# Optimization experiments

Measured on AMD Instinct MI355X. Metric: run time of the kernel, lower is better.

## Reference

```python
import jax, jax.numpy as jnp
import numpy as np

QKV_DIM = 256
C = 32
N_HEAD = 8
OUT_DIM = 256
B1, B2, N = 1, 128, 256


def setup_inputs() -> dict:
    key = jax.random.key(0)
    ks = jax.random.split(key, 8)
    hc = N_HEAD * C
    return {
        "in_data": jax.random.normal(ks[0], (B1, B2, N, QKV_DIM), jnp.float32),
        "mask": jnp.ones((B1, B2, N), jnp.float32),
        "nonbatched_bias": jax.random.normal(ks[1], (B1, N_HEAD, N, N), jnp.float32),
        "w_qkv": jax.random.normal(ks[2], (3 * hc, QKV_DIM), jnp.float32) * (1.0 / np.sqrt(QKV_DIM)),
        "w_gate": jax.random.normal(ks[3], (hc, QKV_DIM), jnp.float32) * 0.02,
        "gating_bias": jnp.ones((hc,), jnp.float32),
        "w_o": jax.random.normal(ks[4], (OUT_DIM, hc), jnp.float32) * 0.02,
        "b_o": jnp.zeros((OUT_DIM,), jnp.float32),
    }


def reference(in_data, mask, nonbatched_bias, w_qkv, w_gate, gating_bias, w_o, b_o):
    scaling = C ** (-0.5)
    # fused QKV projection: [b1,b2,n,3*h*c]
    qkv = jnp.einsum("abnd,ed->abne", in_data, w_qkv)
    q, k, v = jnp.split(qkv, 3, axis=-1)

    def to_heads(t):  # b1 b2 n (h d) -> b1 b2 h n d
        b1, b2, n, _ = t.shape
        return t.reshape(b1, b2, n, N_HEAD, C).transpose(0, 1, 3, 2, 4)

    q, k, v = to_heads(q) * scaling, to_heads(k), to_heads(v)
    # logits: [b1,b2,h,q,k]
    logits = jnp.einsum("abhqd,abhkd->abhqk", q, k)
    mask_bias = (mask[:, :, None, None, :] - 1.0) * 1e9
    logits = logits + mask_bias + nonbatched_bias[:, None]  # broadcast bias over b2
    weights = jax.nn.softmax(logits, axis=-1)
    weighted_avg = jnp.einsum("abhqk,abhkd->abhqd", weights, v)
    b1, b2, h, n, d = weighted_avg.shape
    weighted_avg = weighted_avg.transpose(0, 1, 3, 2, 4).reshape(b1, b2, n, h * d)
    # sigmoid gating
    gate = jax.nn.sigmoid(jnp.einsum("abnd,ed->abne", in_data, w_gate) + gating_bias)
    weighted_avg = gate * weighted_avg
    return jnp.einsum("abne,oe->abno", weighted_avg, w_o) + b_o
```

## Files before the change

### kernel.cpp

```cpp
#include <hip/hip_runtime.h>
#include <hip/hip_bf16.h>
#include <math.h>

#define B2      128
#define NSEQ    256
#define DMODEL  256
#define NHEAD   8
#define CDIM    32
#define HC      256
#define NROWS   (B2*NSEQ)
#define SCALING 0.17677669529663687f

typedef __attribute__((ext_vector_type(8))) short bf16x8;
typedef __attribute__((ext_vector_type(4))) float f32x4;

static __device__ __forceinline__ ushort f2bf(float f) {
    __hip_bfloat16 b = __float2bfloat16(f);
    ushort r; __builtin_memcpy(&r, &b, 2); return r;
}
static __device__ __forceinline__ ushort f2bf_fast(float f) {
    uint u = __builtin_bit_cast(uint, f);
    return (ushort)((u + 0x8000u) >> 16);
}
static __device__ __forceinline__ uint fpack2(float a, float b) {
    const uint ua = __builtin_bit_cast(uint, a) + 0x8000u;
    const uint ub = __builtin_bit_cast(uint, b) + 0x8000u;
    return (ua >> 16) | (ub & 0xFFFF0000u);
}
static __device__ __forceinline__ float bf2f(ushort u) {
    __hip_bfloat16 b; __builtin_memcpy(&b, &u, 2); return __bfloat162float(b);
}
static __device__ __forceinline__ void gload_lds16(const void* g, void* l) {
    __builtin_amdgcn_global_load_lds((const __attribute__((address_space(1))) void*)g,
                                     (__attribute__((address_space(3))) void*)l, 16, 0, 0);
}

#define SWZ(c) ((((c) >> 2) & 3) << 5)

__global__ __launch_bounds__(256) void convertW_kernel(
    const float* __restrict__ Wqkv, const float* __restrict__ Wg,
    const float* __restrict__ Wo,
    ushort* __restrict__ wqkvgb, ushort* __restrict__ wob)
{
    const int NQ = 196608 / 4, NG = 65536 / 4, NO = 65536 / 4;
    const int idx = blockIdx.x * 256 + threadIdx.x;
    const float* src; ushort* dst; int off; float scale = 1.0f;
    if (idx < NQ)           { src = Wqkv; dst = wqkvgb;          off = idx;
                              if (off < 16384) scale = SCALING; }
    else if (idx < NQ + NG) { src = Wg;   dst = wqkvgb + 196608; off = idx - NQ; }
    else                    { src = Wo;   dst = wob;             off = idx - NQ - NG; }
    float4 v = ((const float4*)src)[off];
    union { ushort u[4]; uint2 q; } p;
    p.u[0] = f2bf(v.x * scale); p.u[1] = f2bf(v.y * scale);
    p.u[2] = f2bf(v.z * scale); p.u[3] = f2bf(v.w * scale);
    *(uint2*)(dst + (size_t)off * 4) = p.q;
}

__global__ __launch_bounds__(512, 4) void fused_attn_kernel(
    const float* __restrict__ X,
    const ushort* __restrict__ Wb,
    const float* __restrict__ gbias,
    const float* __restrict__ bias,
    const float* __restrict__ mask,
    ushort* __restrict__ wa_ws)
{
    __shared__ ushort S[40960];

    const int tid  = threadIdx.x;
    const int sid  = (blockIdx.x & 7) * 128 + (blockIdx.x >> 3);
    const int b2   = sid >> 3;
    const int h    = sid & 7;
    const int w    = tid >> 6;
    const int lane = tid & 63;
    const int lj   = lane & 15;
    const int lg   = lane >> 4;
    const int xsl  = ((lg ^ ((lj >> 1) & 3)) << 3);

    {
        const int row  = tid >> 2;
        const int slot = tid & 3;
        const int g8   = (slot ^ ((row >> 1) & 3)) * 8;
        const int wrow = (row < 96) ? ((row >> 5) * 256 + h * 32 + (row & 31))
                                    : (768 + h * 32 + (row & 31));
        const ushort* wsrc = Wb + (size_t)wrow * 256 + g8;
        char* wdst = (char*)S + row * 64 + slot * 16;
        #pragma unroll
        for (int c = 0; c < 8; ++c)
            gload_lds16(wsrc + c * 32, wdst + c * 8192);
    }

    ushort* const Xls = S + 32768;
    const int xrow = tid >> 1;
    const int s2   = (tid & 1) * 2;
    const int rotx = (xrow >> 1) & 3;
    const float* xsrc = X + ((size_t)(b2 * 256 + xrow)) * 256;
    const int g8a = (s2 ^ rotx) * 8;
    const int g8b = ((s2 + 1) ^ rotx) * 8;
    ushort* const xd = Xls + xrow * 32;

    float4 xa0, xa1, xb0, xb1;
    #define XFETCH(t) do {                                          \
        xa0 = *(const float4*)(xsrc + (t) * 32 + g8a);              \
        xa1 = *(const float4*)(xsrc + (t) * 32 + g8a + 4);          \
        xb0 = *(const float4*)(xsrc + (t) * 32 + g8b);              \
        xb1 = *(const float4*)(xsrc + (t) * 32 + g8b + 4);          \
    } while (0)

    XFETCH(0);

    f32x4 acc[4][2][2];
    #pragma unroll
    for (int o = 0; o < 4; ++o)
        #pragma unroll
        for (int eo = 0; eo < 2; ++eo)
            #pragma unroll
            for (int mi = 0; mi < 2; ++mi)
                acc[o][eo][mi] = (f32x4){0.f, 0.f, 0.f, 0.f};

    #pragma unroll
    for (int t = 0; t < 8; ++t) {
        uint4 p0, p1;
        p0.x = fpack2(xa0.x, xa0.y); p0.y = fpack2(xa0.z, xa0.w);
        p0.z = fpack2(xa1.x, xa1.y); p0.w = fpack2(xa1.z, xa1.w);
        p1.x = fpack2(xb0.x, xb0.y); p1.y = fpack2(xb0.z, xb0.w);
        p1.z = fpack2(xb1.x, xb1.y); p1.w = fpack2(xb1.z, xb1.w);
        *(uint4*)(xd + s2 * 8)       = p0;
        *(uint4*)(xd + (s2 + 1) * 8) = p1;
        if (t < 7) XFETCH(t + 1);
        __syncthreads();
        const ushort* Wc = S + t * 4096;
        bf16x8 xv0 = *(const bf16x8*)(Xls + (w * 32 + lj) * 32 + xsl);
        bf16x8 xv1 = *(const bf16x8*)(Xls + (w * 32 + 16 + lj) * 32 + xsl);
        #pragma unroll
        for (int o = 0; o < 4; ++o) {
            const bf16x8 wb0 = *(const bf16x8*)(Wc + (o * 32 + lj) * 32 + xsl);
            const bf16x8 wb1 = *(const bf16x8*)(Wc + (o * 32 + 16 + lj) * 32 + xsl);
            acc[o][0][0] = __builtin_amdgcn_mfma_f32_16x16x32_bf16(wb0, xv0, acc[o][0][0], 0, 0, 0);
            acc[o][0][1] = __builtin_amdgcn_mfma_f32_16x16x32_bf16(wb0, xv1, acc[o][0][1], 0, 0, 0);
            acc[o][1][0] = __builtin_amdgcn_mfma_f32_16x16x32_bf16(wb1, xv0, acc[o][1][0], 0, 0, 0);
            acc[o][1][1] = __builtin_amdgcn_mfma_f32_16x16x32_bf16(wb1, xv1, acc[o][1][1], 0, 0, 0);
        }
        __syncthreads();
    }
    #undef XFETCH

    ushort* const Qb = S;
    ushort* const Kb = S + 8192;
    ushort* const Vb = S + 16384;
    ushort* const Gb = S + 24576;
    {
        const int rot = (lj >> 1) & 3;
        #pragma unroll
        for (int eo = 0; eo < 2; ++eo) {
            const int c0 = eo * 16 + lg * 4;
            const int sl = (((eo * 2 + (lg >> 1)) ^ rot) << 3) + (lg & 1) * 4;
            #pragma unroll
            for (int mi = 0; mi < 2; ++mi) {
                const int n = w * 32 + mi * 16 + lj;
                {
                    const f32x4 v = acc[0][eo][mi];
                    uint2 pk; pk.x = fpack2(v[0], v[1]); pk.y = fpack2(v[2], v[3]);
                    *(uint2*)(Qb + n * 32 + sl) = pk;
                }
                {
                    const f32x4 v = acc[1][eo][mi];
                    uint2 pk; pk.x = fpack2(v[0], v[1]); pk.y = fpack2(v[2], v[3]);
                    *(uint2*)(Kb + n * 32 + sl) = pk;
                }
                {
                    const f32x4 v = acc[3][eo][mi];
                    const float z0 = v[0] + gbias[h * 32 + c0 + 0];
                    const float z1 = v[1] + gbias[h * 32 + c0 + 1];
                    const float z2 = v[2] + gbias[h * 32 + c0 + 2];
                    const float z3 = v[3] + gbias[h * 32 + c0 + 3];
                    uint2 pk;
                    pk.x = fpack2(1.f / (1.f + __expf(-z0)), 1.f / (1.f + __expf(-z1)));
                    pk.y = fpack2(1.f / (1.f + __expf(-z2)), 1.f / (1.f + __expf(-z3)));
                    *(uint2*)(Gb + n * 32 + sl) = pk;
                }
                {
                    #pragma unroll
                    for (int r = 0; r < 4; ++r) {
                        const int c = c0 + r;
                        const int byte = c * 512 + ((2 * n) ^ SWZ(c));
                        Vb[byte >> 1] = f2bf_fast(acc[2][eo][mi][r]);
                    }
                }
            }
        }
    }
    __syncthreads();

    ushort* const PlW = S + 32768 + w * 1024;
    const float* bbase = bias + (size_t)h * 65536;
    const float* mrow  = mask + (size_t)b2 * 256;

    #pragma unroll
    for (int half = 0; half < 2; ++half) {
        const int q0 = w * 32 + half * 16;
        const bf16x8 qf = *(const bf16x8*)(Qb + (q0 + lj) * 32 + xsl);

        f32x4 a2[16];
        #pragma unroll
        for (int t = 0; t < 16; ++t) {
            const int col = t * 16 + lj;
            const float mterm = (mrow[col] - 1.0f) * 1e9f;
            #pragma unroll
            for (int r = 0; r < 4; ++r)
                a2[t][r] = bbase[(size_t)(q0 + lg * 4 + r) * 256 + col] + mterm;
        }

        #pragma unroll
        for (int t = 0; t < 16; ++t) {
            const bf16x8 kf = *(const bf16x8*)(Kb + (t * 16 + lj) * 32 + xsl);
            a2[t] = __builtin_amdgcn_mfma_f32_16x16x32_bf16(qf, kf, a2[t], 0, 0, 0);
        }

        float sr[4] = {0.f, 0.f, 0.f, 0.f};
        #pragma unroll
        for (int t = 0; t < 16; ++t)
            #pragma unroll
            for (int r = 0; r < 4; ++r) {
                const float e = __expf(a2[t][r]);
                a2[t][r] = e;
                sr[r] += e;
            }
        float inv[4];
        #pragma unroll
        for (int r = 0; r < 4; ++r) {
            float s = sr[r];
            s += __shfl_xor(s, 1);
            s += __shfl_xor(s, 2);
            s += __shfl_xor(s, 4);
            s += __shfl_xor(s, 8);
            inv[r] = 1.0f / s;
        }

        f32x4 o0 = {0.f, 0.f, 0.f, 0.f};
        f32x4 o1 = {0.f, 0.f, 0.f, 0.f};
        #pragma unroll
        for (int ch = 0; ch < 4; ++ch) {
            #pragma unroll
            for (int tt = 0; tt < 4; ++tt) {
                const int t = ch * 4 + tt;
                #pragma unroll
                for (int r = 0; r < 4; ++r) {
                    const int row  = lg * 4 + r;
                    const int byte = row * 128 + ((32 * tt + 2 * lj) ^ (lg << 5));
                    PlW[byte >> 1] = f2bf_fast(a2[t][r]);
                }
            }
            #pragma unroll
            for (int kk = 0; kk < 2; ++kk) {
                const int abyte = lj * 128 + ((64 * kk + 16 * lg) ^ SWZ(lj));
                const bf16x8 pa = *(const bf16x8*)(PlW + (abyte >> 1));
                const int ks = ch * 2 + kk;
                {
                    const int cr = lj;
                    const int vbyte = cr * 512 + ((64 * ks + 16 * lg) ^ SWZ(cr));
                    const bf16x8 vb = *(const bf16x8*)(Vb + (vbyte >> 1));
                    o0 = __builtin_amdgcn_mfma_f32_16x16x32_bf16(pa, vb, o0, 0, 0, 0);
                }
                {
                    const int cr = 16 + lj;
                    const int vbyte = cr * 512 + ((64 * ks + 16 * lg) ^ SWZ(cr));
                    const bf16x8 vb = *(const bf16x8*)(Vb + (vbyte >> 1));
                    o1 = __builtin_amdgcn_mfma_f32_16x16x32_bf16(pa, vb, o1, 0, 0, 0);
                }
            }
        }

        #pragma unroll
        for (int r = 0; r < 4; ++r) {
            const int n = q0 + lg * 4 + r;
            const int rotg = ((lg * 4 + r) >> 1) & 3;
            const size_t rowbase = ((size_t)(b2 * 256 + n)) * 256 + h * 32;
            {
                const float gv = bf2f(Gb[n * 32 + (((lj >> 3) ^ rotg) << 3) + (lj & 7)]);
                wa_ws[rowbase + lj] = f2bf_fast(o0[r] * inv[r] * gv);
            }
            {
                const float gv = bf2f(Gb[n * 32 + ((((lj >> 3) + 2) ^ rotg) << 3) + (lj & 7)]);
                wa_ws[rowbase + 16 + lj] = f2bf_fast(o1[r] * inv[r] * gv);
            }
        }
    }
}

__global__ __launch_bounds__(256) void out_mfma_kernel(
    const ushort* __restrict__ WA,
    const ushort* __restrict__ Wob,
    const float* __restrict__ bo,
    float* __restrict__ out)
{
    __shared__ ushort S[20480];
    ushort* const Obuf[2] = { S,        S + 10240 };
    ushort* const Abuf[2] = { S + 8192, S + 18432 };

    const int tid  = threadIdx.x;
    const int w    = tid >> 6;
    const int lane = tid & 63;
    const int lj   = lane & 15;
    const int lg   = lane >> 4;
    const int m0   = blockIdx.x * 64;

    f32x4 acc[4][4];
    #pragma unroll
    for (int i = 0; i < 4; ++i)
        #pragma unroll
        for (int j = 0; j < 4; ++j) acc[i][j] = (f32x4){0.f, 0.f, 0.f, 0.f};

    const int srow = lane >> 2;
    const int scol = (((lane & 3) ^ ((lane >> 3) & 3)) << 3);
    const int xsl  = ((lg ^ ((lj >> 1) & 3)) << 3);

    #define OSTAGE(Odst, Adst, kk) do {                                          \
        _Pragma("unroll")                                                        \
        for (int c = 0; c < 4; ++c) {                                            \
            const int ci = w * 4 + c;                                            \
            gload_lds16(Wob + (size_t)(ci * 16 + srow) * 256 + (kk) + scol,      \
                        (char*)(Odst) + ci * 1024);                              \
        }                                                                        \
        gload_lds16(WA + (size_t)(m0 + w * 16 + srow) * 256 + (kk) + scol,       \
                    (char*)(Adst) + w * 1024);                                   \
    } while (0)

    OSTAGE(Obuf[0], Abuf[0], 0);
    asm volatile("s_waitcnt vmcnt(0)" ::: "memory");
    __builtin_amdgcn_s_barrier();

    #pragma unroll
    for (int t = 0; t < 8; ++t) {
        ushort* Oc = Obuf[t & 1];
        ushort* Ac = Abuf[t & 1];
        if (t < 7) OSTAGE(Obuf[(t + 1) & 1], Abuf[(t + 1) & 1], (t + 1) * 32);
        bf16x8 af[4], bfr[4];
        #pragma unroll
        for (int i = 0; i < 4; ++i)
            af[i] = *(const bf16x8*)(Ac + (i * 16 + lj) * 32 + xsl);
        #pragma unroll
        for (int j = 0; j < 4; ++j)
            bfr[j] = *(const bf16x8*)(Oc + (w * 64 + j * 16 + lj) * 32 + xsl);
        #pragma unroll
        for (int i = 0; i < 4; ++i)
            #pragma unroll
            for (int j = 0; j < 4; ++j)
                acc[i][j] = __builtin_amdgcn_mfma_f32_16x16x32_bf16(af[i], bfr[j], acc[i][j], 0, 0, 0);
        asm volatile("s_waitcnt vmcnt(0)" ::: "memory");
        __builtin_amdgcn_s_barrier();
    }
    #undef OSTAGE

    #pragma unroll
    for (int i = 0; i < 4; ++i) {
        #pragma unroll
        for (int r = 0; r < 4; ++r) {
            const int m = m0 + i * 16 + lg * 4 + r;
            #pragma unroll
            for (int j = 0; j < 4; ++j) {
                const int o = w * 64 + j * 16 + lj;
                out[(size_t)m * 256 + o] = acc[i][j][r] + bo[o];
            }
        }
    }
}

extern "C" void kernel_launch(void* const* d_in, const int* in_sizes, int n_in,
                              void* d_out, int out_size, void* d_ws, size_t ws_size,
                              hipStream_t stream) {
    const float* in_data = (const float*)d_in[0];
    const float* mask    = (const float*)d_in[1];
    const float* nb_bias = (const float*)d_in[2];
    const float* w_qkv   = (const float*)d_in[3];
    const float* w_gate  = (const float*)d_in[4];
    const float* g_bias  = (const float*)d_in[5];
    const float* w_o     = (const float*)d_in[6];
    const float* b_o     = (const float*)d_in[7];
    float* out = (float*)d_out;

    ushort* ws = (ushort*)d_ws;
    ushort* wa_ws  = ws;
    ushort* wqkvgb = wa_ws + (size_t)NROWS * HC;
    ushort* wob    = wqkvgb + 1024 * 256;

    convertW_kernel<<<dim3(320), 256, 0, stream>>>(
        w_qkv, w_gate, w_o, wqkvgb, wob);

    fused_attn_kernel<<<dim3(B2 * NHEAD), 512, 0, stream>>>(
        in_data, wqkvgb, g_bias, nb_bias, mask, wa_ws);

    out_mfma_kernel<<<dim3(NROWS / 64), 256, 0, stream>>>(
        wa_ws, wob, b_o, out);
}
```

Baseline: 85.99 us.

## Load X fragments directly into registers and prefetch bias before barrier

The X tile is now read from global memory straight into the MFMA operand layout and converted to bf16 in registers, so the LDS staging and the two per-iteration __syncthreads in the projection loop go away. The bias and mask loads for the first query half are issued before the projection epilogue barrier so their latency overlaps with it. The later __syncthreads is replaced by an explicit lgkmcnt wait plus s_barrier. In exchange, each lane issues strided, partly uncoalesced global loads of X, and the early a2 prefetch adds register pressure.

```diff
diff --git a/kernel.cpp b/kernel.cpp
--- a/kernel.cpp
+++ b/kernel.cpp
@@ -89,24 +89,16 @@
             gload_lds16(wsrc + c * 32, wdst + c * 8192);
     }
 
-    ushort* const Xls = S + 32768;
-    const int xrow = tid >> 1;
-    const int s2   = (tid & 1) * 2;
-    const int rotx = (xrow >> 1) & 3;
-    const float* xsrc = X + ((size_t)(b2 * 256 + xrow)) * 256;
-    const int g8a = (s2 ^ rotx) * 8;
-    const int g8b = ((s2 + 1) ^ rotx) * 8;
-    ushort* const xd = Xls + xrow * 32;
-
-    float4 xa0, xa1, xb0, xb1;
-    #define XFETCH(t) do {                                          \
-        xa0 = *(const float4*)(xsrc + (t) * 32 + g8a);              \
-        xa1 = *(const float4*)(xsrc + (t) * 32 + g8a + 4);          \
-        xb0 = *(const float4*)(xsrc + (t) * 32 + g8b);              \
-        xb1 = *(const float4*)(xsrc + (t) * 32 + g8b + 4);          \
+    const float* xrow0 = X + ((size_t)(b2 * 256 + w * 32 + lj)) * 256 + lg * 8;
+    const float* xrow1 = xrow0 + 16 * 256;
+    float4 xf00, xf01, xf10, xf11;
+    #define XLOAD(t) do {                                       \
+        xf00 = *(const float4*)(xrow0 + (t) * 32);              \
+        xf01 = *(const float4*)(xrow0 + (t) * 32 + 4);          \
+        xf10 = *(const float4*)(xrow1 + (t) * 32);              \
+        xf11 = *(const float4*)(xrow1 + (t) * 32 + 4);          \
     } while (0)
-
-    XFETCH(0);
+    XLOAD(0);
 
     f32x4 acc[4][2][2];
     #pragma unroll
@@ -117,20 +109,19 @@
             for (int mi = 0; mi < 2; ++mi)
                 acc[o][eo][mi] = (f32x4){0.f, 0.f, 0.f, 0.f};
 
+    __syncthreads();
+
     #pragma unroll
     for (int t = 0; t < 8; ++t) {
-        uint4 p0, p1;
-        p0.x = fpack2(xa0.x, xa0.y); p0.y = fpack2(xa0.z, xa0.w);
-        p0.z = fpack2(xa1.x, xa1.y); p0.w = fpack2(xa1.z, xa1.w);
-        p1.x = fpack2(xb0.x, xb0.y); p1.y = fpack2(xb0.z, xb0.w);
-        p1.z = fpack2(xb1.x, xb1.y); p1.w = fpack2(xb1.z, xb1.w);
-        *(uint4*)(xd + s2 * 8)       = p0;
-        *(uint4*)(xd + (s2 + 1) * 8) = p1;
-        if (t < 7) XFETCH(t + 1);
-        __syncthreads();
+        union { uint4 u; bf16x8 b; } cv0, cv1;
+        cv0.u.x = fpack2(xf00.x, xf00.y); cv0.u.y = fpack2(xf00.z, xf00.w);
+        cv0.u.z = fpack2(xf01.x, xf01.y); cv0.u.w = fpack2(xf01.z, xf01.w);
+        cv1.u.x = fpack2(xf10.x, xf10.y); cv1.u.y = fpack2(xf10.z, xf10.w);
+        cv1.u.z = fpack2(xf11.x, xf11.y); cv1.u.w = fpack2(xf11.z, xf11.w);
+        const bf16x8 xv0 = cv0.b;
+        const bf16x8 xv1 = cv1.b;
+        if (t < 7) XLOAD(t + 1);
         const ushort* Wc = S + t * 4096;
-        bf16x8 xv0 = *(const bf16x8*)(Xls + (w * 32 + lj) * 32 + xsl);
-        bf16x8 xv1 = *(const bf16x8*)(Xls + (w * 32 + 16 + lj) * 32 + xsl);
         #pragma unroll
         for (int o = 0; o < 4; ++o) {
             const bf16x8 wb0 = *(const bf16x8*)(Wc + (o * 32 + lj) * 32 + xsl);
@@ -140,9 +131,25 @@
             acc[o][1][0] = __builtin_amdgcn_mfma_f32_16x16x32_bf16(wb1, xv0, acc[o][1][0], 0, 0, 0);
             acc[o][1][1] = __builtin_amdgcn_mfma_f32_16x16x32_bf16(wb1, xv1, acc[o][1][1], 0, 0, 0);
         }
-        __syncthreads();
-    }
-    #undef XFETCH
+    }
+    #undef XLOAD
+
+    const float* bbase = bias + (size_t)h * 65536;
+    const float* mrow  = mask + (size_t)b2 * 256;
+    f32x4 a2[16];
+    {
+        const int q0 = w * 32;
+        #pragma unroll
+        for (int t = 0; t < 16; ++t) {
+            const int col = t * 16 + lj;
+            const float mterm = (mrow[col] - 1.0f) * 1e9f;
+            #pragma unroll
+            for (int r = 0; r < 4; ++r)
+                a2[t][r] = bbase[(size_t)(q0 + lg * 4 + r) * 256 + col] + mterm;
+        }
+    }
+
+    __builtin_amdgcn_s_barrier();
 
     ushort* const Qb = S;
     ushort* const Kb = S + 8192;
@@ -189,26 +196,25 @@
             }
         }
     }
-    __syncthreads();
+    asm volatile("s_waitcnt lgkmcnt(0)" ::: "memory");
+    __builtin_amdgcn_s_barrier();
 
     ushort* const PlW = S + 32768 + w * 1024;
-    const float* bbase = bias + (size_t)h * 65536;
-    const float* mrow  = mask + (size_t)b2 * 256;
 
     #pragma unroll
     for (int half = 0; half < 2; ++half) {
         const int q0 = w * 32 + half * 16;
+        if (half == 1) {
+            #pragma unroll
+            for (int t = 0; t < 16; ++t) {
+                const int col = t * 16 + lj;
+                const float mterm = (mrow[col] - 1.0f) * 1e9f;
+                #pragma unroll
+                for (int r = 0; r < 4; ++r)
+                    a2[t][r] = bbase[(size_t)(q0 + lg * 4 + r) * 256 + col] + mterm;
+            }
+        }
         const bf16x8 qf = *(const bf16x8*)(Qb + (q0 + lj) * 32 + xsl);
-
-        f32x4 a2[16];
-        #pragma unroll
-        for (int t = 0; t < 16; ++t) {
-            const int col = t * 16 + lj;
-            const float mterm = (mrow[col] - 1.0f) * 1e9f;
-            #pragma unroll
-            for (int r = 0; r < 4; ++r)
-                a2[t][r] = bbase[(size_t)(q0 + lg * 4 + r) * 256 + col] + mterm;
-        }
 
         #pragma unroll
         for (int t = 0; t < 16; ++t) {
```

Measured after the change: 112.7 us. +31.1%, slower.
